# Kernel optimization log

Measured on AMD Instinct MI355X. Metric: run time of the kernel, lower is better.

Reference implementation:

```python
import jax, jax.numpy as jnp
import numpy as np

N, D, H, C, OUT = 50000, 128, 2, 128, 2   # nodes, in-feat, heads, per-head width, classes
E = 800000
HC = H * C
NEG_SLOPE = 0.2


def setup_inputs() -> dict:
    key = jax.random.key(0)
    ks = jax.random.split(key, 12)
    x = jax.random.normal(ks[0], (N, D), dtype=jnp.float32)
    edge_index = jax.random.randint(ks[1], (2, E), 0, N, dtype=jnp.int64)
    def w(k, fan_in, shape):
        return jax.random.normal(k, shape, dtype=jnp.float32) / np.sqrt(fan_in)
    return {
        "x": x,
        "edge_index": edge_index,
        # layer 0: in D -> H*C
        "W0": w(ks[2], D, (D, HC)),
        "att_src0": w(ks[3], C, (H, C)),
        "att_dst0": w(ks[4], C, (H, C)),
        "b0": jnp.zeros((HC,), dtype=jnp.float32),
        # layer 1: in H*C -> H*C
        "W1": w(ks[5], HC, (HC, HC)),
        "att_src1": w(ks[6], C, (H, C)),
        "att_dst1": w(ks[7], C, (H, C)),
        "b1": jnp.zeros((HC,), dtype=jnp.float32),
        # final linear: H*C -> OUT (concat GAT output)
        "Wl": w(ks[8], HC, (HC, OUT)),
        "bl": jnp.zeros((OUT,), dtype=jnp.float32),
    }


def _gat_layer(x, src, dst, W, att_src, att_dst, b):
    """PyG GATConv (concat=True, negative_slope=0.2, self-loops already in src/dst)."""
    n = x.shape[0]
    h = (x @ W).reshape(n, H, C)                       # [N,H,C]
    a_s = jnp.einsum("nhc,hc->nh", h, att_src)         # [N,H]
    a_d = jnp.einsum("nhc,hc->nh", h, att_dst)         # [N,H]
    logits = jax.nn.leaky_relu(a_s[src] + a_d[dst], NEG_SLOPE)  # [E',H]
    m = jax.ops.segment_max(logits, dst, num_segments=n)
    e = jnp.exp(logits - m[dst])
    denom = jax.ops.segment_sum(e, dst, num_segments=n)
    alpha = e / (denom[dst] + 1e-16)                   # softmax over incoming edges
    msg = h[src] * alpha[:, :, None]                   # [E',H,C]
    out = jax.ops.segment_sum(msg, dst, num_segments=n)
    return out.reshape(n, HC) + b


def reference(x, edge_index, W0, att_src0, att_dst0, b0,
              W1, att_src1, att_dst1, b1, Wl, bl):
    n = x.shape[0]
    loop = jnp.arange(n, dtype=edge_index.dtype)
    src = jnp.concatenate([edge_index[0], loop])       # add self loops (GATConv default)
    dst = jnp.concatenate([edge_index[1], loop])
    h = _gat_layer(x, src, dst, W0, att_src0, att_dst0, b0)
    h = jnp.tanh(h)                                    # tanh between layers only
    h = _gat_layer(h, src, dst, W1, att_src1, att_dst1, b1)
    out = h @ Wl + bl
    return jax.nn.softmax(out, axis=1)
```

## Files before the change

### kernel.cpp

```cpp
#include <hip/hip_runtime.h>
#include <math.h>

constexpr int N_NODES = 50000;
constexpr int N_EDGES = 800000;
constexpr int TOT_E   = N_EDGES + N_NODES;
constexpr int HCv     = 256;
constexpr int MAXD    = 256;

constexpr int GB32 = (N_NODES + 31) / 32;

constexpr int PADSH = 5;

constexpr int PREP_CVT  = (N_NODES * 128 / 4 + 255) / 256;
constexpr int PREP_WT0  = 128;
constexpr int PREP_DEG  = (TOT_E + 255) / 256;
constexpr int PREP_ZA   = (N_NODES * 8 / 4 + 255) / 256;
constexpr int PREP_SKIN = (N_NODES + 15) / 16;
constexpr int PREP_C    = 1;
constexpr int PREP_BLKS = PREP_CVT + PREP_WT0 + PREP_DEG + PREP_ZA + PREP_SKIN + PREP_C;

typedef __attribute__((ext_vector_type(8))) short bf16x8;
typedef __attribute__((ext_vector_type(4))) float f32x4;
typedef __attribute__((ext_vector_type(2))) float f32x2;

__device__ __forceinline__ unsigned short f2bf(float f) {
    unsigned int u = __float_as_uint(f);
    unsigned int r = (u + 0x7fffu + ((u >> 16) & 1u)) >> 16;
    return (unsigned short)r;
}
__device__ __forceinline__ unsigned int f2bf_pack(float lo, float hi) {
    return (unsigned int)f2bf(lo) | ((unsigned int)f2bf(hi) << 16);
}
__device__ __forceinline__ float bf2f_lo(unsigned int packed) {
    return __uint_as_float(packed << 16);
}
__device__ __forceinline__ float bf2f_hi(unsigned int packed) {
    return __uint_as_float(packed & 0xffff0000u);
}

__device__ __forceinline__ float lrelu(float x) { return x > 0.f ? x : 0.2f * x; }


__global__ __launch_bounds__(256) void zero_pre_k(uint4* __restrict__ degp4,
        int* __restrict__ total, float* __restrict__ c2,
        const float* __restrict__ W0, const float* __restrict__ att_src0,
        const float* __restrict__ att_dst0,
        const float* __restrict__ W1, const float* __restrict__ att_src1,
        const float* __restrict__ att_dst1, const float* __restrict__ Wl,
        float* __restrict__ w0buf, float* __restrict__ pv) {
    int i = blockIdx.x * blockDim.x + threadIdx.x;
    if (i < N_NODES * 32 / 4) degp4[i] = make_uint4(0, 0, 0, 0);
    if (blockIdx.x == 0) {
        if (threadIdx.x == 0) { *total = 0; c2[0] = 0.f; c2[1] = 0.f; }
        int k = threadIdx.x;
        float v0 = 0, v1 = 0, v2 = 0, v3 = 0, v4 = 0, v5 = 0, v6 = 0, v7 = 0;
        const float* wr = W1 + (size_t)k * 256;
        for (int c = 0; c < 128; ++c) {
            float wv = wr[c];
            v0 = fmaf(wv, att_src1[c], v0);
            v2 = fmaf(wv, att_dst1[c], v2);
            v4 = fmaf(wv, Wl[c * 2 + 0], v4);
            v5 = fmaf(wv, Wl[c * 2 + 1], v5);
        }
        for (int c = 128; c < 256; ++c) {
            float wv = wr[c];
            v1 = fmaf(wv, att_src1[c], v1);
            v3 = fmaf(wv, att_dst1[c], v3);
            v6 = fmaf(wv, Wl[c * 2 + 0], v6);
            v7 = fmaf(wv, Wl[c * 2 + 1], v7);
        }
        float* p = pv + (size_t)k * 8;
        p[0] = v0; p[1] = v1; p[2] = v2; p[3] = v3;
        p[4] = v4; p[5] = v5; p[6] = v6; p[7] = v7;
        if (k < 128) {
            float w0v = 0, w1v = 0, w2v = 0, w3v = 0;
            const float* wr0 = W0 + (size_t)k * 256;
            for (int c = 0; c < 128; ++c) {
                float wv = wr0[c];
                w0v = fmaf(wv, att_src0[c], w0v);
                w2v = fmaf(wv, att_dst0[c], w2v);
            }
            for (int c = 128; c < 256; ++c) {
                float wv = wr0[c];
                w1v = fmaf(wv, att_src0[c], w1v);
                w3v = fmaf(wv, att_dst0[c], w3v);
            }
            float* q = w0buf + (size_t)k * 4;
            q[0] = w0v; q[1] = w1v; q[2] = w2v; q[3] = w3v;
        }
    }
}


__global__ __launch_bounds__(256) void prep_k(const float* __restrict__ x,
        unsigned short* __restrict__ xb, const float* __restrict__ W0,
        unsigned short* __restrict__ WT0, const int* __restrict__ ei,
        int* __restrict__ degp, float* __restrict__ asd1,
        const float* __restrict__ w0buf, float* __restrict__ a_s,
        float* __restrict__ a_d, const float* __restrict__ Wl,
        const float* __restrict__ b1, const float* __restrict__ bl,
        float* __restrict__ c2) {
    int b = blockIdx.x;
    if (b < PREP_CVT) {
        int i = b * 256 + threadIdx.x;
        if (i < N_NODES * 128 / 4) {
            float4 v = *reinterpret_cast<const float4*>(x + (size_t)i * 4);
            ushort4 o;
            o.x = f2bf(v.x); o.y = f2bf(v.y); o.z = f2bf(v.z); o.w = f2bf(v.w);
            *reinterpret_cast<ushort4*>(xb + (size_t)i * 4) = o;
        }
        return;
    }
    b -= PREP_CVT;
    if (b < PREP_WT0) {
        int idx = b * 256 + threadIdx.x;
        int k = idx >> 8, n = idx & 255;
        WT0[(size_t)n * 128 + k] = f2bf(W0[idx]);
        return;
    }
    b -= PREP_WT0;
    if (b < PREP_DEG) {
        int e = b * 256 + threadIdx.x;
        if (e < TOT_E) {
            int dst = (e < N_EDGES) ? ei[N_EDGES + e] : (e - N_EDGES);
            atomicAdd(&degp[dst << PADSH], 1);
        }
        return;
    }
    b -= PREP_DEG;
    if (b < PREP_ZA) {
        int i = b * 256 + threadIdx.x;
        if (i < N_NODES * 2)
            *reinterpret_cast<float4*>(asd1 + (size_t)i * 4) = make_float4(0, 0, 0, 0);
        return;
    }
    b -= PREP_ZA;
    if (b < PREP_SKIN) {
        int lane = threadIdx.x & 63;
        int sub = lane >> 4;
        int lq = lane & 15;
        int node = b * 16 + (threadIdx.x >> 6) * 4 + sub;
        if (node < N_NODES) {
            const float* xr = x + (size_t)node * 128 + lq * 8;
            const float4* wv = reinterpret_cast<const float4*>(w0buf) + lq * 8;
            float s0 = 0, s1 = 0, d0 = 0, d1 = 0;
#pragma unroll
            for (int t = 0; t < 8; ++t) {
                float xv = xr[t];
                float4 w = wv[t];
                s0 = fmaf(xv, w.x, s0);
                s1 = fmaf(xv, w.y, s1);
                d0 = fmaf(xv, w.z, d0);
                d1 = fmaf(xv, w.w, d1);
            }
#pragma unroll
            for (int off = 1; off < 16; off <<= 1) {
                s0 += __shfl_xor(s0, off);
                s1 += __shfl_xor(s1, off);
                d0 += __shfl_xor(d0, off);
                d1 += __shfl_xor(d1, off);
            }
            if (lq == 0) {
                *reinterpret_cast<float2*>(a_s + node * 2) = make_float2(s0, s1);
                *reinterpret_cast<float2*>(a_d + node * 2) = make_float2(d0, d1);
            }
        }
        return;
    }
    {
        int k = threadIdx.x;
        int lane = k & 63;
        float bv = b1[k];
        float p0 = bv * Wl[k * 2 + 0];
        float p1 = bv * Wl[k * 2 + 1];
        if (k == 0) { p0 += bl[0]; p1 += bl[1]; }
#pragma unroll
        for (int off = 32; off; off >>= 1) {
            p0 += __shfl_xor(p0, off);
            p1 += __shfl_xor(p1, off);
        }
        if (lane == 0) {
            atomicAdd(&c2[0], p0);
            atomicAdd(&c2[1], p1);
        }
    }
}


__global__ void offsets_k(const int* __restrict__ degp, int* __restrict__ start,
                          int* __restrict__ deg, int* __restrict__ cursorp,
                          int* __restrict__ total) {
    int lane = threadIdx.x & 63;
    int node = blockIdx.x * blockDim.x + threadIdx.x;
    int d = (node < N_NODES) ? degp[node << PADSH] : 0;
    int pre = d;
#pragma unroll
    for (int off = 1; off < 64; off <<= 1) {
        int v = __shfl_up(pre, off);
        if (lane >= off) pre += v;
    }
    int wtot = __shfl(pre, 63);
    int base = 0;
    if (lane == 63) base = atomicAdd(total, wtot);
    base = __shfl(base, 63);
    int my = base + pre - d;
    if (node < N_NODES) {
        start[node] = my;
        deg[node] = d;
        cursorp[node << PADSH] = my;
    }
}

__global__ void scatter_k(const int* __restrict__ ei, int* __restrict__ cursorp,
                          int* __restrict__ colv) {
    int e = blockIdx.x * blockDim.x + threadIdx.x;
    if (e >= TOT_E) return;
    int srcv, dstv;
    if (e < N_EDGES) { srcv = ei[e]; dstv = ei[N_EDGES + e]; }
    else             { srcv = dstv = e - N_EDGES; }
    int pos = atomicAdd(&cursorp[dstv << PADSH], 1);
    colv[pos] = srcv;
}


__global__ __launch_bounds__(256) void agg0x_k(const unsigned short* __restrict__ xb,
                      const float* __restrict__ a_s, const float* __restrict__ a_d,
                      const int* __restrict__ start, const int* __restrict__ deg,
                      const int* __restrict__ colv,
                      unsigned short* __restrict__ xagg) {
    __shared__ float lexp[4][MAXD][2];
    const int lane = threadIdx.x & 63;
    const int wslot = threadIdx.x >> 6;
    const int node = blockIdx.x * 4 + wslot;
    if (node >= N_NODES) return;
    const int beg = start[node];
    const int degv = deg[node];
    const float ad0 = a_d[node * 2], ad1 = a_d[node * 2 + 1];
    const int* __restrict__ col = colv + beg;

    if (degv <= MAXD) {
        float s0 = 0.f, s1 = 0.f;
        for (int j = lane; j < degv; j += 64) {
            int s = col[j];
            float2 av = *reinterpret_cast<const float2*>(a_s + s * 2);
            float e0 = __expf(lrelu(av.x + ad0));
            float e1 = __expf(lrelu(av.y + ad1));
            *reinterpret_cast<float2*>(&lexp[wslot][j][0]) = make_float2(e0, e1);
            s0 += e0;
            s1 += e1;
        }
#pragma unroll
        for (int off = 32; off; off >>= 1) {
            s0 += __shfl_xor(s0, off);
            s1 += __shfl_xor(s1, off);
        }
        const float inv0 = 1.f / (s0 + 1e-16f);
        const float inv1 = 1.f / (s1 + 1e-16f);

        const int q = lane >> 4;
        const int lq = lane & 15;
        const unsigned short* __restrict__ xp = xb + lq * 8;
        f32x2 aA[4] = {};
        f32x2 aB[4] = {};
        const int full = degv >> 2;
        for (int i = 0; i < full; ++i) {
            const int j = 4 * i + q;
            const int s = col[j];
            float2 ee = *reinterpret_cast<float2*>(&lexp[wslot][j][0]);
            const uint4 hv = *reinterpret_cast<const uint4*>(xp + (size_t)s * 128);
            const f32x2 al0 = {ee.x, ee.x};
            const f32x2 al1 = {ee.y, ee.y};
            f32x2 p;
            p.x = bf2f_lo(hv.x); p.y = bf2f_hi(hv.x);
            aA[0] = __builtin_elementwise_fma(p, al0, aA[0]);
            aB[0] = __builtin_elementwise_fma(p, al1, aB[0]);
            p.x = bf2f_lo(hv.y); p.y = bf2f_hi(hv.y);
            aA[1] = __builtin_elementwise_fma(p, al0, aA[1]);
            aB[1] = __builtin_elementwise_fma(p, al1, aB[1]);
            p.x = bf2f_lo(hv.z); p.y = bf2f_hi(hv.z);
            aA[2] = __builtin_elementwise_fma(p, al0, aA[2]);
            aB[2] = __builtin_elementwise_fma(p, al1, aB[2]);
            p.x = bf2f_lo(hv.w); p.y = bf2f_hi(hv.w);
            aA[3] = __builtin_elementwise_fma(p, al0, aA[3]);
            aB[3] = __builtin_elementwise_fma(p, al1, aB[3]);
        }
        {
            const int j = full * 4 + q;
            if (j < degv) {
                const int s = col[j];
                float2 ee = *reinterpret_cast<float2*>(&lexp[wslot][j][0]);
                const uint4 hv = *reinterpret_cast<const uint4*>(xp + (size_t)s * 128);
                const f32x2 al0 = {ee.x, ee.x};
                const f32x2 al1 = {ee.y, ee.y};
                f32x2 p;
                p.x = bf2f_lo(hv.x); p.y = bf2f_hi(hv.x);
                aA[0] = __builtin_elementwise_fma(p, al0, aA[0]);
                aB[0] = __builtin_elementwise_fma(p, al1, aB[0]);
                p.x = bf2f_lo(hv.y); p.y = bf2f_hi(hv.y);
                aA[1] = __builtin_elementwise_fma(p, al0, aA[1]);
                aB[1] = __builtin_elementwise_fma(p, al1, aB[1]);
                p.x = bf2f_lo(hv.z); p.y = bf2f_hi(hv.z);
                aA[2] = __builtin_elementwise_fma(p, al0, aA[2]);
                aB[2] = __builtin_elementwise_fma(p, al1, aB[2]);
                p.x = bf2f_lo(hv.w); p.y = bf2f_hi(hv.w);
                aA[3] = __builtin_elementwise_fma(p, al0, aA[3]);
                aB[3] = __builtin_elementwise_fma(p, al1, aB[3]);
            }
        }
        float acc[16];
#pragma unroll
        for (int c = 0; c < 4; ++c) {
            acc[2 * c]     = aA[c].x;
            acc[2 * c + 1] = aA[c].y;
            acc[8 + 2 * c]     = aB[c].x;
            acc[8 + 2 * c + 1] = aB[c].y;
        }
#pragma unroll
        for (int c = 0; c < 16; ++c) {
            acc[c] += __shfl_xor(acc[c], 16);
            acc[c] += __shfl_xor(acc[c], 32);
        }
        if (lane < 16) {
#pragma unroll
            for (int c = 0; c < 8; ++c)  acc[c] *= inv0;
#pragma unroll
            for (int c = 8; c < 16; ++c) acc[c] *= inv1;
            uint4 v0, v1;
            v0.x = f2bf_pack(acc[0], acc[1]);
            v0.y = f2bf_pack(acc[2], acc[3]);
            v0.z = f2bf_pack(acc[4], acc[5]);
            v0.w = f2bf_pack(acc[6], acc[7]);
            v1.x = f2bf_pack(acc[8], acc[9]);
            v1.y = f2bf_pack(acc[10], acc[11]);
            v1.z = f2bf_pack(acc[12], acc[13]);
            v1.w = f2bf_pack(acc[14], acc[15]);
            *reinterpret_cast<uint4*>(xagg + (size_t)node * 256 + lq * 8) = v0;
            *reinterpret_cast<uint4*>(xagg + (size_t)node * 256 + 128 + lq * 8) = v1;
        }
    } else {
        const int end = beg + degv;
        float m0 = -INFINITY, m1 = -INFINITY;
        for (int e = beg + lane; e < end; e += 64) {
            int s = colv[e];
            m0 = fmaxf(m0, lrelu(a_s[s * 2] + ad0));
            m1 = fmaxf(m1, lrelu(a_s[s * 2 + 1] + ad1));
        }
#pragma unroll
        for (int off = 32; off; off >>= 1) {
            m0 = fmaxf(m0, __shfl_xor(m0, off));
            m1 = fmaxf(m1, __shfl_xor(m1, off));
        }
        float s0 = 0.f, s1 = 0.f;
        for (int e = beg + lane; e < end; e += 64) {
            int s = colv[e];
            s0 += __expf(lrelu(a_s[s * 2] + ad0) - m0);
            s1 += __expf(lrelu(a_s[s * 2 + 1] + ad1) - m1);
        }
#pragma unroll
        for (int off = 32; off; off >>= 1) {
            s0 += __shfl_xor(s0, off);
            s1 += __shfl_xor(s1, off);
        }
        float inv0 = 1.f / (s0 + 1e-16f);
        float inv1 = 1.f / (s1 + 1e-16f);
        const int cbase = lane * 2;
        float a00 = 0.f, a01 = 0.f, a10 = 0.f, a11 = 0.f;
        for (int e = beg; e < end; ++e) {
            int s = colv[e];
            float2 av = *reinterpret_cast<const float2*>(a_s + s * 2);
            float al0 = __expf(lrelu(av.x + ad0) - m0) * inv0;
            float al1 = __expf(lrelu(av.y + ad1) - m1) * inv1;
            unsigned int xv = *reinterpret_cast<const unsigned int*>(
                xb + (size_t)s * 128 + cbase);
            float x0 = bf2f_lo(xv), x1 = bf2f_hi(xv);
            a00 = fmaf(x0, al0, a00);
            a01 = fmaf(x1, al0, a01);
            a10 = fmaf(x0, al1, a10);
            a11 = fmaf(x1, al1, a11);
        }
        *reinterpret_cast<unsigned int*>(xagg + (size_t)node * 256 + cbase) =
            f2bf_pack(a00, a01);
        *reinterpret_cast<unsigned int*>(xagg + (size_t)node * 256 + 128 + cbase) =
            f2bf_pack(a10, a11);
    }
}


__global__ __launch_bounds__(256) void gemm_tanh_k(
        const unsigned short* __restrict__ A,
        const unsigned short* __restrict__ BT,
        const float* __restrict__ b0,
        const float* __restrict__ pv,
        float* __restrict__ asd1, int M) {
    __shared__ float sh[2][32][8];
    const int gy = blockIdx.x;
    const int lane = threadIdx.x & 63;
    const int wv = threadIdx.x >> 6;
    const int head = wv >> 1;
    const int rh = wv & 1;
    const int lm = lane & 15;
    const int g8 = (lane >> 4) * 8;
    const int row0 = gy * 32 + rh * 16;

    int ra = row0 + lm;
    if (ra >= M) ra = M - 1;
    const unsigned short* pa = A + (size_t)ra * 256 + head * 128 + g8;
    const unsigned short* pb = BT + (size_t)(head * 128 + lm) * 128 + g8;

    f32x4 acc[8] = {};
#pragma unroll
    for (int kt = 0; kt < 128; kt += 32) {
        bf16x8 a0 = *reinterpret_cast<const bf16x8*>(pa + kt);
#pragma unroll
        for (int j = 0; j < 8; ++j) {
            bf16x8 bf = *reinterpret_cast<const bf16x8*>(
                pb + (size_t)j * 16 * 128 + kt);
            acc[j] = __builtin_amdgcn_mfma_f32_16x16x32_bf16(a0, bf, acc[j], 0, 0, 0);
        }
    }

    float pr[8][4];
#pragma unroll
    for (int p = 0; p < 8; ++p)
#pragma unroll
        for (int r = 0; r < 4; ++r) pr[p][r] = 0.f;
#pragma unroll
    for (int j = 0; j < 8; ++j) {
        const int c = head * 128 + j * 16 + lm;
        const float bc = b0[c];
        const float4 pA = *reinterpret_cast<const float4*>(pv + (size_t)c * 8);
        const float4 pB = *reinterpret_cast<const float4*>(pv + (size_t)c * 8 + 4);
#pragma unroll
        for (int r = 0; r < 4; ++r) {
            float th = tanhf(acc[j][r] + bc);
            pr[0][r] = fmaf(th, pA.x, pr[0][r]);
            pr[1][r] = fmaf(th, pA.y, pr[1][r]);
            pr[2][r] = fmaf(th, pA.z, pr[2][r]);
            pr[3][r] = fmaf(th, pA.w, pr[3][r]);
            pr[4][r] = fmaf(th, pB.x, pr[4][r]);
            pr[5][r] = fmaf(th, pB.y, pr[5][r]);
            pr[6][r] = fmaf(th, pB.z, pr[6][r]);
            pr[7][r] = fmaf(th, pB.w, pr[7][r]);
        }
    }
#pragma unroll
    for (int off = 1; off < 16; off <<= 1)
#pragma unroll
        for (int p = 0; p < 8; ++p)
#pragma unroll
            for (int r = 0; r < 4; ++r)
                pr[p][r] += __shfl_xor(pr[p][r], off);
    if (lm == 0) {
        int lrow = rh * 16 + (lane >> 4) * 4;
#pragma unroll
        for (int r = 0; r < 4; ++r)
#pragma unroll
            for (int p = 0; p < 8; ++p)
                sh[head][lrow + r][p] = pr[p][r];
    }
    __syncthreads();

    if (threadIdx.x < 64) {
        int row = threadIdx.x >> 1;
        int half = threadIdx.x & 1;
        int grow = gy * 32 + row;
        if (grow < M) {
            float4 v;
            v.x = sh[0][row][half * 4 + 0] + sh[1][row][half * 4 + 0];
            v.y = sh[0][row][half * 4 + 1] + sh[1][row][half * 4 + 1];
            v.z = sh[0][row][half * 4 + 2] + sh[1][row][half * 4 + 2];
            v.w = sh[0][row][half * 4 + 3] + sh[1][row][half * 4 + 3];
            *reinterpret_cast<float4*>(asd1 + (size_t)grow * 8 + half * 4) = v;
        }
    }
}


__global__ __launch_bounds__(256) void agg_final_k(
        const float* __restrict__ asd1, const int* __restrict__ start,
        const int* __restrict__ deg, const int* __restrict__ colv,
        const float* __restrict__ c2, float* __restrict__ out) {
    const int lane = threadIdx.x & 63;
    const int node = blockIdx.x * 4 + (threadIdx.x >> 6);
    if (node >= N_NODES) return;
    const int beg = start[node];
    const int degv = deg[node];
    const float ad0 = asd1[node * 8 + 2];
    const float ad1v = asd1[node * 8 + 3];
    const int* __restrict__ col = colv + beg;

    float s0 = 0.f, s1 = 0.f, A00 = 0.f, A01 = 0.f, A10 = 0.f, A11 = 0.f;
    for (int j = lane; j < degv; j += 64) {
        int s = col[j];
        const float* rs = asd1 + (size_t)s * 8;
        float2 av = *reinterpret_cast<const float2*>(rs);
        float4 gv = *reinterpret_cast<const float4*>(rs + 4);
        float e0 = __expf(lrelu(av.x + ad0));
        float e1 = __expf(lrelu(av.y + ad1v));
        s0 += e0;
        s1 += e1;
        A00 = fmaf(e0, gv.x, A00);
        A01 = fmaf(e0, gv.y, A01);
        A10 = fmaf(e1, gv.z, A10);
        A11 = fmaf(e1, gv.w, A11);
    }
#pragma unroll
    for (int off = 32; off; off >>= 1) {
        s0  += __shfl_xor(s0, off);
        s1  += __shfl_xor(s1, off);
        A00 += __shfl_xor(A00, off);
        A01 += __shfl_xor(A01, off);
        A10 += __shfl_xor(A10, off);
        A11 += __shfl_xor(A11, off);
    }
    if (lane == 0) {
        float i0 = 1.f / (s0 + 1e-16f), i1 = 1.f / (s1 + 1e-16f);
        float z0 = A00 * i0 + A10 * i1 + c2[0];
        float z1 = A01 * i0 + A11 * i1 + c2[1];
        float mx = fmaxf(z0, z1);
        float e0 = __expf(z0 - mx), e1 = __expf(z1 - mx);
        float inv = 1.f / (e0 + e1);
        out[node * 2 + 0] = e0 * inv;
        out[node * 2 + 1] = e1 * inv;
    }
}


extern "C" void kernel_launch(void* const* d_in, const int* in_sizes, int n_in,
                              void* d_out, int out_size, void* d_ws, size_t ws_size,
                              hipStream_t stream) {
    const float* x        = (const float*)d_in[0];
    const int*   ei       = (const int*)d_in[1];
    const float* W0       = (const float*)d_in[2];
    const float* att_src0 = (const float*)d_in[3];
    const float* att_dst0 = (const float*)d_in[4];
    const float* b0       = (const float*)d_in[5];
    const float* W1       = (const float*)d_in[6];
    const float* att_src1 = (const float*)d_in[7];
    const float* att_dst1 = (const float*)d_in[8];
    const float* b1       = (const float*)d_in[9];
    const float* Wl       = (const float*)d_in[10];
    const float* bl       = (const float*)d_in[11];
    float* out = (float*)d_out;

    unsigned short* xb   = (unsigned short*)d_ws;
    unsigned short* xagg = xb + (size_t)N_NODES * 128;
    unsigned short* WT0  = xagg + (size_t)N_NODES * 256;
    float* w0buf = (float*)(WT0 + 256 * 128);
    float* pv    = w0buf + 128 * 4;
    float* as0   = pv + 256 * 8;
    float* ad0   = as0 + N_NODES * 2;
    float* asd1  = ad0 + N_NODES * 2;
    int*   degp  = (int*)(asd1 + (size_t)N_NODES * 8);
    int* cursorp = degp + (size_t)N_NODES * 32;
    int* deg     = cursorp + (size_t)N_NODES * 32;
    int* start   = deg + N_NODES;
    int* total   = start + N_NODES;
    float* c2    = (float*)(total + 1);
    int* colv    = (int*)(c2 + 2);

    zero_pre_k<<<(N_NODES * 32 / 4 + 255) / 256, 256, 0, stream>>>(
        (uint4*)degp, total, c2, W0, att_src0, att_dst0,
        W1, att_src1, att_dst1, Wl, w0buf, pv);

    prep_k<<<PREP_BLKS, 256, 0, stream>>>(x, xb, W0, WT0, ei, degp, asd1,
                                          w0buf, as0, ad0, Wl, b1, bl, c2);

    offsets_k<<<(N_NODES + 255) / 256, 256, 0, stream>>>(degp, start, deg, cursorp, total);
    scatter_k<<<(TOT_E + 255) / 256, 256, 0, stream>>>(ei, cursorp, colv);

    int nn4 = (N_NODES + 3) / 4;

    agg0x_k<<<nn4, 256, 0, stream>>>(xb, as0, ad0, start, deg, colv, xagg);
    gemm_tanh_k<<<GB32, 256, 0, stream>>>(xagg, WT0, b0, pv, asd1, N_NODES);

    agg_final_k<<<nn4, 256, 0, stream>>>(asd1, start, deg, colv, c2, out);
}
```

Before: 265.0 us.

## Fuse layer-0 aggregation with W0 projection, tanh and attention scores

The separate MFMA GEMM+tanh kernel is removed. Each wavefront now stages its aggregated node row in shared memory and multiplies it by bf16 W0 using scalar FMAs, then applies tanh and the attention projections and writes asd1 directly. This drops the xagg round trip through global memory and one kernel launch. In exchange the dense GEMM moves from matrix cores to per-lane FMA loops that read W0 from cache for every node, which may make compute or cache bandwidth the bottleneck.

```diff
diff --git a/kernel.cpp b/kernel.cpp
--- a/kernel.cpp
+++ b/kernel.cpp
@@ -4,20 +4,16 @@
 constexpr int N_NODES = 50000;
 constexpr int N_EDGES = 800000;
 constexpr int TOT_E   = N_EDGES + N_NODES;
-constexpr int HCv     = 256;
 constexpr int MAXD    = 256;
 
-constexpr int GB32 = (N_NODES + 31) / 32;
-
 constexpr int PADSH = 5;
 
 constexpr int PREP_CVT  = (N_NODES * 128 / 4 + 255) / 256;
-constexpr int PREP_WT0  = 128;
+constexpr int PREP_W0B  = 128;
 constexpr int PREP_DEG  = (TOT_E + 255) / 256;
-constexpr int PREP_ZA   = (N_NODES * 8 / 4 + 255) / 256;
 constexpr int PREP_SKIN = (N_NODES + 15) / 16;
 constexpr int PREP_C    = 1;
-constexpr int PREP_BLKS = PREP_CVT + PREP_WT0 + PREP_DEG + PREP_ZA + PREP_SKIN + PREP_C;
+constexpr int PREP_BLKS = PREP_CVT + PREP_W0B + PREP_DEG + PREP_SKIN + PREP_C;
 
 typedef __attribute__((ext_vector_type(8))) short bf16x8;
 typedef __attribute__((ext_vector_type(4))) float f32x4;
@@ -94,8 +90,8 @@
 
 __global__ __launch_bounds__(256) void prep_k(const float* __restrict__ x,
         unsigned short* __restrict__ xb, const float* __restrict__ W0,
-        unsigned short* __restrict__ WT0, const int* __restrict__ ei,
-        int* __restrict__ degp, float* __restrict__ asd1,
+        unsigned short* __restrict__ W0b, const int* __restrict__ ei,
+        int* __restrict__ degp,
         const float* __restrict__ w0buf, float* __restrict__ a_s,
         float* __restrict__ a_d, const float* __restrict__ Wl,
         const float* __restrict__ b1, const float* __restrict__ bl,
@@ -112,13 +108,12 @@
         return;
     }
     b -= PREP_CVT;
-    if (b < PREP_WT0) {
+    if (b < PREP_W0B) {
         int idx = b * 256 + threadIdx.x;
-        int k = idx >> 8, n = idx & 255;
-        WT0[(size_t)n * 128 + k] = f2bf(W0[idx]);
+        W0b[idx] = f2bf(W0[idx]);
         return;
     }
-    b -= PREP_WT0;
+    b -= PREP_W0B;
     if (b < PREP_DEG) {
         int e = b * 256 + threadIdx.x;
         if (e < TOT_E) {
@@ -128,13 +123,6 @@
         return;
     }
     b -= PREP_DEG;
-    if (b < PREP_ZA) {
-        int i = b * 256 + threadIdx.x;
-        if (i < N_NODES * 2)
-            *reinterpret_cast<float4*>(asd1 + (size_t)i * 4) = make_float4(0, 0, 0, 0);
-        return;
-    }
-    b -= PREP_ZA;
     if (b < PREP_SKIN) {
         int lane = threadIdx.x & 63;
         int sub = lane >> 4;
@@ -227,8 +215,12 @@
                       const float* __restrict__ a_s, const float* __restrict__ a_d,
                       const int* __restrict__ start, const int* __restrict__ deg,
                       const int* __restrict__ colv,
-                      unsigned short* __restrict__ xagg) {
+                      const unsigned short* __restrict__ W0b,
+                      const float* __restrict__ b0,
+                      const float* __restrict__ pv,
+                      float* __restrict__ asd1) {
     __shared__ float lexp[4][MAXD][2];
+    __shared__ float xsh[4][2][128];
     const int lane = threadIdx.x & 63;
     const int wslot = threadIdx.x >> 6;
     const int node = blockIdx.x * 4 + wslot;
@@ -322,20 +314,10 @@
         }
         if (lane < 16) {
 #pragma unroll
-            for (int c = 0; c < 8; ++c)  acc[c] *= inv0;
-#pragma unroll
-            for (int c = 8; c < 16; ++c) acc[c] *= inv1;
-            uint4 v0, v1;
-            v0.x = f2bf_pack(acc[0], acc[1]);
-            v0.y = f2bf_pack(acc[2], acc[3]);
-            v0.z = f2bf_pack(acc[4], acc[5]);
-            v0.w = f2bf_pack(acc[6], acc[7]);
-            v1.x = f2bf_pack(acc[8], acc[9]);
-            v1.y = f2bf_pack(acc[10], acc[11]);
-            v1.z = f2bf_pack(acc[12], acc[13]);
-            v1.w = f2bf_pack(acc[14], acc[15]);
-            *reinterpret_cast<uint4*>(xagg + (size_t)node * 256 + lq * 8) = v0;
-            *reinterpret_cast<uint4*>(xagg + (size_t)node * 256 + 128 + lq * 8) = v1;
+            for (int c = 0; c < 8; ++c) {
+                xsh[wslot][0][lq * 8 + c] = acc[c] * inv0;
+                xsh[wslot][1][lq * 8 + c] = acc[8 + c] * inv1;
+            }
         }
     } else {
         const int end = beg + degv;
@@ -378,100 +360,55 @@
             a10 = fmaf(x0, al1, a10);
             a11 = fmaf(x1, al1, a11);
         }
-        *reinterpret_cast<unsigned int*>(xagg + (size_t)node * 256 + cbase) =
-            f2bf_pack(a00, a01);
-        *reinterpret_cast<unsigned int*>(xagg + (size_t)node * 256 + 128 + cbase) =
-            f2bf_pack(a10, a11);
-    }
-}
-
-
-__global__ __launch_bounds__(256) void gemm_tanh_k(
-        const unsigned short* __restrict__ A,
-        const unsigned short* __restrict__ BT,
-        const float* __restrict__ b0,
-        const float* __restrict__ pv,
-        float* __restrict__ asd1, int M) {
-    __shared__ float sh[2][32][8];
-    const int gy = blockIdx.x;
-    const int lane = threadIdx.x & 63;
-    const int wv = threadIdx.x >> 6;
-    const int head = wv >> 1;
-    const int rh = wv & 1;
-    const int lm = lane & 15;
-    const int g8 = (lane >> 4) * 8;
-    const int row0 = gy * 32 + rh * 16;
-
-    int ra = row0 + lm;
-    if (ra >= M) ra = M - 1;
-    const unsigned short* pa = A + (size_t)ra * 256 + head * 128 + g8;
-    const unsigned short* pb = BT + (size_t)(head * 128 + lm) * 128 + g8;
-
-    f32x4 acc[8] = {};
-#pragma unroll
-    for (int kt = 0; kt < 128; kt += 32) {
-        bf16x8 a0 = *reinterpret_cast<const bf16x8*>(pa + kt);
-#pragma unroll
-        for (int j = 0; j < 8; ++j) {
-            bf16x8 bf = *reinterpret_cast<const bf16x8*>(
-                pb + (size_t)j * 16 * 128 + kt);
-            acc[j] = __builtin_amdgcn_mfma_f32_16x16x32_bf16(a0, bf, acc[j], 0, 0, 0);
-        }
-    }
-
-    float pr[8][4];
-#pragma unroll
-    for (int p = 0; p < 8; ++p)
-#pragma unroll
-        for (int r = 0; r < 4; ++r) pr[p][r] = 0.f;
-#pragma unroll
-    for (int j = 0; j < 8; ++j) {
-        const int c = head * 128 + j * 16 + lm;
-        const float bc = b0[c];
-        const float4 pA = *reinterpret_cast<const float4*>(pv + (size_t)c * 8);
-        const float4 pB = *reinterpret_cast<const float4*>(pv + (size_t)c * 8 + 4);
-#pragma unroll
-        for (int r = 0; r < 4; ++r) {
-            float th = tanhf(acc[j][r] + bc);
-            pr[0][r] = fmaf(th, pA.x, pr[0][r]);
-            pr[1][r] = fmaf(th, pA.y, pr[1][r]);
-            pr[2][r] = fmaf(th, pA.z, pr[2][r]);
-            pr[3][r] = fmaf(th, pA.w, pr[3][r]);
-            pr[4][r] = fmaf(th, pB.x, pr[4][r]);
-            pr[5][r] = fmaf(th, pB.y, pr[5][r]);
-            pr[6][r] = fmaf(th, pB.z, pr[6][r]);
-            pr[7][r] = fmaf(th, pB.w, pr[7][r]);
-        }
-    }
-#pragma unroll
-    for (int off = 1; off < 16; off <<= 1)
+        xsh[wslot][0][cbase]     = a00;
+        xsh[wslot][0][cbase + 1] = a01;
+        xsh[wslot][1][cbase]     = a10;
+        xsh[wslot][1][cbase + 1] = a11;
+    }
+
+    const int head = lane >> 5;
+    const int c4 = (lane & 31) * 4 + head * 128;
+    const float* __restrict__ xv = &xsh[wslot][head][0];
+    const unsigned short* __restrict__ wp = W0b + c4;
+    float h0 = 0.f, h1 = 0.f, h2 = 0.f, h3 = 0.f;
+#pragma unroll 8
+    for (int k = 0; k < 128; ++k) {
+        float xk = xv[k];
+        uint2 wv4 = *reinterpret_cast<const uint2*>(wp + (size_t)k * 256);
+        h0 = fmaf(bf2f_lo(wv4.x), xk, h0);
+        h1 = fmaf(bf2f_hi(wv4.x), xk, h1);
+        h2 = fmaf(bf2f_lo(wv4.y), xk, h2);
+        h3 = fmaf(bf2f_hi(wv4.y), xk, h3);
+    }
+    const float4 bb = *reinterpret_cast<const float4*>(b0 + c4);
+    float th[4];
+    th[0] = tanhf(h0 + bb.x);
+    th[1] = tanhf(h1 + bb.y);
+    th[2] = tanhf(h2 + bb.z);
+    th[3] = tanhf(h3 + bb.w);
+    float pr[8] = {};
+#pragma unroll
+    for (int r = 0; r < 4; ++r) {
+        const float4 pA = *reinterpret_cast<const float4*>(pv + (size_t)(c4 + r) * 8);
+        const float4 pB = *reinterpret_cast<const float4*>(pv + (size_t)(c4 + r) * 8 + 4);
+        pr[0] = fmaf(th[r], pA.x, pr[0]);
+        pr[1] = fmaf(th[r], pA.y, pr[1]);
+        pr[2] = fmaf(th[r], pA.z, pr[2]);
+        pr[3] = fmaf(th[r], pA.w, pr[3]);
+        pr[4] = fmaf(th[r], pB.x, pr[4]);
+        pr[5] = fmaf(th[r], pB.y, pr[5]);
+        pr[6] = fmaf(th[r], pB.z, pr[6]);
+        pr[7] = fmaf(th[r], pB.w, pr[7]);
+    }
+#pragma unroll
+    for (int off = 1; off < 64; off <<= 1)
 #pragma unroll
         for (int p = 0; p < 8; ++p)
-#pragma unroll
-            for (int r = 0; r < 4; ++r)
-                pr[p][r] += __shfl_xor(pr[p][r], off);
-    if (lm == 0) {
-        int lrow = rh * 16 + (lane >> 4) * 4;
-#pragma unroll
-        for (int r = 0; r < 4; ++r)
-#pragma unroll
-            for (int p = 0; p < 8; ++p)
-                sh[head][lrow + r][p] = pr[p][r];
-    }
-    __syncthreads();
-
-    if (threadIdx.x < 64) {
-        int row = threadIdx.x >> 1;
-        int half = threadIdx.x & 1;
-        int grow = gy * 32 + row;
-        if (grow < M) {
-            float4 v;
-            v.x = sh[0][row][half * 4 + 0] + sh[1][row][half * 4 + 0];
-            v.y = sh[0][row][half * 4 + 1] + sh[1][row][half * 4 + 1];
-            v.z = sh[0][row][half * 4 + 2] + sh[1][row][half * 4 + 2];
-            v.w = sh[0][row][half * 4 + 3] + sh[1][row][half * 4 + 3];
-            *reinterpret_cast<float4*>(asd1 + (size_t)grow * 8 + half * 4) = v;
-        }
+            pr[p] += __shfl_xor(pr[p], off);
+    if (lane == 0) {
+        float4* dst = reinterpret_cast<float4*>(asd1 + (size_t)node * 8);
+        dst[0] = make_float4(pr[0], pr[1], pr[2], pr[3]);
+        dst[1] = make_float4(pr[4], pr[5], pr[6], pr[7]);
     }
 }
 
@@ -544,9 +481,8 @@
     float* out = (float*)d_out;
 
     unsigned short* xb   = (unsigned short*)d_ws;
-    unsigned short* xagg = xb + (size_t)N_NODES * 128;
-    unsigned short* WT0  = xagg + (size_t)N_NODES * 256;
-    float* w0buf = (float*)(WT0 + 256 * 128);
+    unsigned short* W0b  = xb + (size_t)N_NODES * 128;
+    float* w0buf = (float*)(W0b + 128 * 256);
     float* pv    = w0buf + 128 * 4;
     float* as0   = pv + 256 * 8;
     float* ad0   = as0 + N_NODES * 2;
@@ -563,7 +499,7 @@
         (uint4*)degp, total, c2, W0, att_src0, att_dst0,
         W1, att_src1, att_dst1, Wl, w0buf, pv);
 
-    prep_k<<<PREP_BLKS, 256, 0, stream>>>(x, xb, W0, WT0, ei, degp, asd1,
+    prep_k<<<PREP_BLKS, 256, 0, stream>>>(x, xb, W0, W0b, ei, degp,
                                           w0buf, as0, ad0, Wl, b1, bl, c2);
 
     offsets_k<<<(N_NODES + 255) / 256, 256, 0, stream>>>(degp, start, deg, cursorp, total);
@@ -571,8 +507,8 @@
 
     int nn4 = (N_NODES + 3) / 4;
 
-    agg0x_k<<<nn4, 256, 0, stream>>>(xb, as0, ad0, start, deg, colv, xagg);
-    gemm_tanh_k<<<GB32, 256, 0, stream>>>(xagg, WT0, b0, pv, asd1, N_NODES);
+    agg0x_k<<<nn4, 256, 0, stream>>>(xb, as0, ad0, start, deg, colv,
+                                     W0b, b0, pv, asd1);
 
     agg_final_k<<<nn4, 256, 0, stream>>>(asd1, start, deg, colv, c2, out);
 }
```

Result: slower. 400.5 us (+51.1%).
